# Kernel optimization log

Measured on AMD Instinct MI355X. Metric: run time of the kernel, lower is better.

## Reference

```python
import jax, jax.numpy as jnp
import numpy as np

D = 512
H = 2048
L = 8192
NSEG = 16
LN_EPS = 1e-6  # flax LayerNorm default


def _ln_tokens(x):
    # flax LayerNorm(reduction_axes=-2, feature_axes=-1, use_bias=False, use_scale=False):
    # mean/var reduced over the token axis (-2), per feature; no learned params.
    mu = jnp.mean(x, axis=-2, keepdims=True)
    var = jnp.var(x, axis=-2, keepdims=True)
    return (x - mu) * jax.lax.rsqrt(var + LN_EPS)


def setup_inputs() -> dict:
    key = jax.random.key(0)
    ks = jax.random.split(key, 8)
    xcat = jax.random.normal(ks[0], (L, D), dtype=jnp.float32)
    xsep = jnp.sort(jax.random.randint(ks[1], (L,), 0, NSEG)).astype(jnp.int64)
    s = 0.02
    Wqkv = jax.random.normal(ks[2], (D, 3 * D), dtype=jnp.float32) * s
    bqkv = jnp.zeros((3 * D,), dtype=jnp.float32)
    W1 = jax.random.normal(ks[3], (D, H), dtype=jnp.float32) * s
    b1 = jnp.zeros((H,), dtype=jnp.float32)
    W2 = jax.random.normal(ks[4], (H, D), dtype=jnp.float32) * s
    b2 = jnp.zeros((D,), dtype=jnp.float32)
    return {"xcat": xcat, "xsep": xsep, "Wqkv": Wqkv, "bqkv": bqkv,
            "W1": W1, "b1": b1, "W2": W2, "b2": b2}


def reference(xcat, xsep, Wqkv, bqkv, W1, b1, W2, b2):
    Ltok = xcat.shape[0]
    qkv = _ln_tokens(xcat) @ Wqkv + bqkv            # [L, 3D]
    q = qkv[:, :D]
    k = qkv[:, D:2 * D]
    # v = qkv[:, 2*D:3*D]  # computed in original but never used
    # unscaled scores; softmax FIRST, then mask, then renormalize (faithful to source)
    atten = jax.nn.softmax(jnp.einsum('id,jd->ij', q, k), axis=-1)  # [L, L]
    idx = jnp.arange(Ltok)
    mask = (xsep[None, :] == xsep[:, None]) & (idx[None, :] <= idx[:, None])
    atten = atten * mask
    atten = atten / (atten.sum(axis=-1, keepdims=True) + 1e-10)
    ctx = atten @ xcat                               # attention applied to raw xcat
    ffn = jax.nn.relu(_ln_tokens(ctx) @ W1 + b1) @ W2 + b2
    return (xcat + ffn, xsep)
```

## Files before the change

### kernel.cpp

```cpp
#include <hip/hip_runtime.h>
#include <math.h>

#define LTOK 8192
#define DDIM 512
#define HDIM 2048
#define NSEG 16
#define DCUT 32
#define ZROWS (NSEG * DCUT)
#define ZCH 64
#define NPART (ZCH * 4)
#define BM 128
#define BN 128
#define BK 64
#define PW 1280
#define PTILES (PW / BN)
#define ZGB (ZCH * (ZROWS / BM))
#define SPB (PTILES * 64)
#define ZG_PER (ZGB / 128)
#define SP_PER (SPB / 128)
#define GRP_SZ (ZG_PER + SP_PER)

typedef float f32x4 __attribute__((ext_vector_type(4)));
typedef short s16x8 __attribute__((ext_vector_type(8)));

static __device__ __forceinline__ short f2bf(float f) {
    union { float f; unsigned u; } v; v.f = f;
    unsigned r = (v.u + 0x7fffu + ((v.u >> 16) & 1u)) >> 16;
    return (short)r;
}
static __device__ __forceinline__ float bf2f(short s) {
    union { unsigned u; float f; } v;
    v.u = ((unsigned)(unsigned short)s) << 16;
    return v.f;
}

template<int GX, int GY>
__device__ __forceinline__ void swz_yslow(int& x, int& y) {
    constexpr int cpx = (GX * GY) >> 3;
    const int orig = blockIdx.y * GX + blockIdx.x;
    const int lg = (orig & 7) * cpx + (orig >> 3);
    y = lg / GX;
    x = lg - y * GX;
}

__global__ void ln_stats_partial(const float* __restrict__ X,
                                 float* __restrict__ psum, float* __restrict__ psumsq) {
    int c = threadIdx.x;
    int b = blockIdx.x;
    const float* p = X + (size_t)b * 256 * DDIM + c;
    float s = 0.f, s2 = 0.f;
    for (int r = 0; r < 256; ++r) {
        float v = p[(size_t)r * DDIM];
        s += v; s2 += v * v;
    }
    psum[b * DDIM + c] = s;
    psumsq[b * DDIM + c] = s2;
}

__global__ void ln_stats_final(const float* __restrict__ psum, const float* __restrict__ psumsq,
                               float* __restrict__ mu, float* __restrict__ rstd, int nb) {
    int c = threadIdx.x;
    float s = 0.f, s2 = 0.f;
    for (int b = 0; b < nb; ++b) { s += psum[b * DDIM + c]; s2 += psumsq[b * DDIM + c]; }
    float m = s / (float)LTOK;
    float var = s2 / (float)LTOK - m * m;
    mu[c] = m;
    rstd[c] = rsqrtf(var + 1e-6f);
}

__global__ void ln_apply_bf16(const float* __restrict__ X,
                              const float* __restrict__ mu, const float* __restrict__ rstd,
                              short* __restrict__ out) {
    int t = blockIdx.x * 256 + threadIdx.x;
    int base = t * 4;
    int c = base & (DDIM - 1);
    float4 v = *(const float4*)(X + base);
    short4 o;
    o.x = f2bf((v.x - mu[c + 0]) * rstd[c + 0]);
    o.y = f2bf((v.y - mu[c + 1]) * rstd[c + 1]);
    o.z = f2bf((v.z - mu[c + 2]) * rstd[c + 2]);
    o.w = f2bf((v.w - mu[c + 3]) * rstd[c + 3]);
    *(short4*)(out + base) = o;
}

__global__ void transpose_w(const float* __restrict__ W, int ldw, int n0,
                            short* __restrict__ WT, int R) {
    __shared__ short t[32][33];
    int nb = n0 + blockIdx.x * 32;
    int rb = blockIdx.y * 32;
    int tx = threadIdx.x & 31, ty = threadIdx.x >> 5;
    for (int rr = ty; rr < 32; rr += 8)
        t[rr][tx] = f2bf(W[(size_t)(rb + rr) * ldw + nb + tx]);
    __syncthreads();
    for (int rr = ty; rr < 32; rr += 8)
        WT[(size_t)(nb - n0 + rr) * R + rb + tx] = t[tx][rr];
}

__global__ void transpose_bf16(const float* __restrict__ X, short* __restrict__ XT) {
    __shared__ short t[32][33];
    int c0 = blockIdx.x * 32;
    int r0 = blockIdx.y * 32;
    int tx = threadIdx.x & 31, ty = threadIdx.x >> 5;
    for (int rr = ty; rr < 32; rr += 8)
        t[rr][tx] = f2bf(X[(size_t)(r0 + rr) * DDIM + c0 + tx]);
    __syncthreads();
    for (int rr = ty; rr < 32; rr += 8)
        XT[(size_t)(c0 + rr) * LTOK + r0 + tx] = t[tx][rr];
}

__global__ void seg_begin_k(const int* __restrict__ sep, int* __restrict__ begin,
                            float* __restrict__ out2) {
    int i = blockIdx.x * 256 + threadIdx.x;
    if (i < LTOK) {
        if (i == 0 || sep[i] != sep[i - 1]) begin[sep[i]] = i;
        out2[i] = (float)sep[i];
    }
}

__global__ void gather_qz(const short* __restrict__ qk, const int* __restrict__ sep,
                          const int* __restrict__ begin, short* __restrict__ qg) {
    const int gi = blockIdx.x;
    const int s = gi / DCUT, d = gi - s * DCUT;
    const int r = begin[s] + d;
    if ((unsigned)r < LTOK && sep[r] == s) {
        const short2* src = (const short2*)(qk + (size_t)r * 1024);
        short2* dst = (short2*)(qg + (size_t)gi * DDIM);
        dst[threadIdx.x] = src[threadIdx.x];
    }
}

__device__ __forceinline__ void stage_tile512(const short* __restrict__ src, int lda,
                                              short* lds, int tid) {
    const int wave = tid >> 6;
    const int lane = tid & 63;
    #pragma unroll
    for (int u = 0; u < 2; ++u) {
        const int c = u * 512 + wave * 64 + lane;
        const short* g = src + (size_t)(c >> 3) * lda + (c & 7) * 8;
        short* l = lds + (size_t)(u * 512 + wave * 64) * 8;
        __builtin_amdgcn_global_load_lds(
            (const __attribute__((address_space(1))) unsigned int*)g,
            (__attribute__((address_space(3))) unsigned int*)l,
            16, 0, 0);
    }
}

__device__ __forceinline__ void mma8_step(const short (*As)[BK], const short (*Bs)[BK],
                                          f32x4 acc[4][2], int wr, int wc, int grp, int lrow) {
    #pragma unroll
    for (int kk = 0; kk < 2; ++kk) {
        s16x8 af[4], bfr[2];
        #pragma unroll
        for (int f = 0; f < 4; ++f)
            af[f] = *(const s16x8*)&As[wr * 64 + f * 16 + lrow][grp * 8 + kk * 32];
        #pragma unroll
        for (int f = 0; f < 2; ++f)
            bfr[f] = *(const s16x8*)&Bs[wc * 32 + f * 16 + lrow][grp * 8 + kk * 32];
        #pragma unroll
        for (int fm = 0; fm < 4; ++fm)
            #pragma unroll
            for (int fn = 0; fn < 2; ++fn)
                acc[fm][fn] = __builtin_amdgcn_mfma_f32_16x16x32_bf16(
                    af[fm], bfr[fn], acc[fm][fn], 0, 0, 0);
    }
}

template<int EPI, int GX, int GY>
__global__ __launch_bounds__(512) void mm_bt8(const short* __restrict__ A, int lda,
        const short* __restrict__ BT, int ldb,
        const float* __restrict__ bias, const float* __restrict__ resid,
        float* __restrict__ Cf, short* __restrict__ Cb, int ldc, int K) {
    __shared__ short As[BM][BK];
    __shared__ short Bs[BN][BK];
    const int tid = threadIdx.x;
    const int wave = tid >> 6, lane = tid & 63, grp = lane >> 4, lrow = lane & 15;
    const int wr = wave >> 2, wc = wave & 3;
    int bx, by;
    swz_yslow<GX, GY>(bx, by);
    const int m0 = by * BM, n0 = bx * BN;
    if (EPI == 3) {
        A += (size_t)blockIdx.z * K;
        BT += (size_t)blockIdx.z * K;
    }
    f32x4 acc[4][2];
    #pragma unroll
    for (int a = 0; a < 4; ++a)
        #pragma unroll
        for (int b = 0; b < 2; ++b) acc[a][b] = (f32x4){0.f, 0.f, 0.f, 0.f};
    for (int k0 = 0; k0 < K; k0 += BK) {
        __syncthreads();
        stage_tile512(A + (size_t)m0 * lda + k0, lda, &As[0][0], tid);
        stage_tile512(BT + (size_t)n0 * ldb + k0, ldb, &Bs[0][0], tid);
        asm volatile("s_waitcnt vmcnt(0)" ::: "memory");
        __syncthreads();
        mma8_step(As, Bs, acc, wr, wc, grp, lrow);
    }
    #pragma unroll
    for (int fm = 0; fm < 4; ++fm) {
        #pragma unroll
        for (int i = 0; i < 4; ++i) {
            int row = m0 + wr * 64 + fm * 16 + grp * 4 + i;
            #pragma unroll
            for (int fn = 0; fn < 2; ++fn) {
                int col = n0 + wc * 32 + fn * 16 + lrow;
                float v = acc[fm][fn][i] + (EPI == 3 ? 0.f : bias[col]);
                if (EPI == 1) v = fmaxf(v, 0.f);
                if (EPI == 2) {
                    Cf[(size_t)row * ldc + col] = v + resid[(size_t)row * ldc + col];
                } else if (EPI == 3) {
                    Cb[(size_t)blockIdx.z * ((size_t)LTOK * ldc)
                       + (size_t)row * ldc + col] = f2bf(v);
                } else {
                    Cb[(size_t)row * ldc + col] = f2bf(v);
                }
            }
        }
    }
}

__global__ void ffn2_combine(const short* __restrict__ hp, const float* __restrict__ b2,
                             const float* __restrict__ xcat, float* __restrict__ out) {
    const int t = blockIdx.x * 256 + threadIdx.x;
    const int base = t * 4;
    const int c = base & (DDIM - 1);
    float4 r = *(const float4*)(xcat + base);
    float4 a;
    a.x = r.x + b2[c + 0];
    a.y = r.y + b2[c + 1];
    a.z = r.z + b2[c + 2];
    a.w = r.w + b2[c + 3];
    #pragma unroll
    for (int z = 0; z < 4; ++z) {
        short4 p = *(const short4*)(hp + (size_t)z * LTOK * DDIM + base);
        a.x += bf2f(p.x); a.y += bf2f(p.y); a.z += bf2f(p.z); a.w += bf2f(p.w);
    }
    *(float4*)(out + base) = a;
}

__global__ __launch_bounds__(512) void attn_zgsp(const short* __restrict__ qg,
        const short* __restrict__ qk,
        const int* __restrict__ sep, const int* __restrict__ begin,
        short* __restrict__ P, float* __restrict__ Zg) {
    __shared__ short As[BM][BK];
    __shared__ short Bs[BN][BK];
    const int tid = threadIdx.x;
    const int wave = tid >> 6, lane = tid & 63, grp = lane >> 4, lrow = lane & 15;
    const int wr = wave >> 2, wc = wave & 3;
    const int bid = blockIdx.x;
    const int grpi = bid / GRP_SZ, rem = bid - grpi * GRP_SZ;
    f32x4 acc[4][2];
    #pragma unroll
    for (int a = 0; a < 4; ++a)
        #pragma unroll
        for (int b = 0; b < 2; ++b) acc[a][b] = (f32x4){0.f, 0.f, 0.f, 0.f};

    if (rem < ZG_PER) {
        const int orig = grpi * ZG_PER + rem;
        constexpr int cpx = ZGB >> 3;
        const int lg = (orig & 7) * cpx + (orig >> 3);
        const int bx = lg / (ZROWS / BM);
        const int by = lg - bx * (ZROWS / BM);
        const int g0 = by * BM;
        const int j0 = bx * BN;
        for (int k0 = 0; k0 < DDIM; k0 += BK) {
            __syncthreads();
            stage_tile512(qg + (size_t)g0 * DDIM + k0, DDIM, &As[0][0], tid);
            stage_tile512(qk + (size_t)j0 * 1024 + 512 + k0, 1024, &Bs[0][0], tid);
            asm volatile("s_waitcnt vmcnt(0)" ::: "memory");
            __syncthreads();
            mma8_step(As, Bs, acc, wr, wc, grp, lrow);
        }
        #pragma unroll
        for (int idx = 0; idx < 16; ++idx) {
            float z = __expf(acc[idx >> 2][0][idx & 3]) + __expf(acc[idx >> 2][1][idx & 3]);
            #pragma unroll
            for (int off = 1; off < 16; off <<= 1) z += __shfl_xor(z, off, 16);
            if (lrow == 0) {
                const int gi = g0 + wr * 64 + (idx >> 2) * 16 + grp * 4 + (idx & 3);
                Zg[(size_t)gi * NPART + bx * 4 + wc] = z;
            }
        }
    } else {
        const int orig = grpi * SP_PER + (rem - ZG_PER);
        constexpr int cpx = SPB >> 3;
        const int lg = (orig & 7) * cpx + (orig >> 3);
        const int by = lg / PTILES;
        const int bx = lg - by * PTILES;
        const int m0 = by * BM;
        const int jb0 = begin[sep[m0]] & ~(BN - 1);
        const int j0 = jb0 + bx * BN;
        if (j0 >= m0 + BM) return;
        for (int k0 = 0; k0 < DDIM; k0 += BK) {
            __syncthreads();
            stage_tile512(qk + (size_t)m0 * 1024 + k0, 1024, &As[0][0], tid);
            stage_tile512(qk + (size_t)j0 * 1024 + 512 + k0, 1024, &Bs[0][0], tid);
            asm volatile("s_waitcnt vmcnt(0)" ::: "memory");
            __syncthreads();
            mma8_step(As, Bs, acc, wr, wc, grp, lrow);
        }
        #pragma unroll
        for (int fm = 0; fm < 4; ++fm) {
            #pragma unroll
            for (int i = 0; i < 4; ++i) {
                const int row = m0 + wr * 64 + fm * 16 + grp * 4 + i;
                const int jsr = begin[sep[row]];
                short* pr = P + (size_t)row * PW + (j0 - jb0) + wc * 32;
                #pragma unroll
                for (int fn = 0; fn < 2; ++fn) {
                    const int col = j0 + wc * 32 + fn * 16 + lrow;
                    const float ez = __expf(acc[fm][fn][i]);
                    pr[fn * 16 + lrow] = f2bf((col >= jsr && col <= row) ? ez : 0.f);
                }
            }
        }
    }
}

__global__ void einv_k(const short* __restrict__ P,
                       const int* __restrict__ sep, const int* __restrict__ begin,
                       const float* __restrict__ Zg, float* __restrict__ invE) {
    const int wv = threadIdx.x >> 6, lane = threadIdx.x & 63;
    const int r = blockIdx.x * 4 + wv;
    const int m0 = r & ~(BM - 1);
    const int jb0 = begin[sep[m0]] & ~(BN - 1);
    const int kw = m0 + BM - jb0;
    const int sr = sep[r];
    const int jsr = begin[sr];
    const short* Pr = P + (size_t)r * PW;
    float e = 0.f;
    for (int c = lane * 2; c < kw; c += 128) {
        short2 v = *(const short2*)(Pr + c);
        e += bf2f(v.x) + bf2f(v.y);
    }
    const int d = r - jsr;
    float z = 0.f;
    if (d < DCUT) {
        const float* zr = Zg + (size_t)(sr * DCUT + d) * NPART;
        #pragma unroll
        for (int c = 0; c < NPART / 64; ++c) z += zr[c * 64 + lane];
    }
    #pragma unroll
    for (int off = 1; off < 64; off <<= 1) {
        e += __shfl_xor(e, off);
        z += __shfl_xor(z, off);
    }
    if (lane == 0) invE[r] = 1.f / (e + 1e-10f * z);
}

__global__ __launch_bounds__(512) void attn_pv(const short* __restrict__ P,
        const short* __restrict__ xbT,
        const int* __restrict__ sep, const int* __restrict__ begin,
        const float* __restrict__ invE, float* __restrict__ ctx,
        float* __restrict__ psum2, float* __restrict__ psumsq2) {
    __shared__ short As[BM][BK];
    __shared__ short Bs[BN][BK];
    __shared__ float Sacc[128][2];
    const int tid = threadIdx.x;
    const int wave = tid >> 6, lane = tid & 63, grp = lane >> 4, lrow = lane & 15;
    const int wr = wave >> 2, wc = wave & 3;
    int bx, by;
    swz_yslow<4, 64>(bx, by);
    const int m0 = by * BM, n0 = bx * BN;
    const int jbase0 = begin[sep[m0]] & ~(BN - 1);
    const int kmax = m0 + BM - jbase0;
    f32x4 acc[4][2];
    #pragma unroll
    for (int a = 0; a < 4; ++a)
        #pragma unroll
        for (int b = 0; b < 2; ++b) acc[a][b] = (f32x4){0.f, 0.f, 0.f, 0.f};
    for (int k0 = 0; k0 < kmax; k0 += BK) {
        __syncthreads();
        stage_tile512(P + (size_t)m0 * PW + k0, PW, &As[0][0], tid);
        stage_tile512(xbT + (size_t)n0 * LTOK + jbase0 + k0, LTOK, &Bs[0][0], tid);
        asm volatile("s_waitcnt vmcnt(0)" ::: "memory");
        __syncthreads();
        mma8_step(As, Bs, acc, wr, wc, grp, lrow);
    }
    if (tid < 128) { Sacc[tid][0] = 0.f; Sacc[tid][1] = 0.f; }
    __syncthreads();
    float cs[2] = {0.f, 0.f}, cq[2] = {0.f, 0.f};
    #pragma unroll
    for (int fm = 0; fm < 4; ++fm) {
        #pragma unroll
        for (int i = 0; i < 4; ++i) {
            int row = m0 + wr * 64 + fm * 16 + grp * 4 + i;
            float inv = invE[row];
            #pragma unroll
            for (int fn = 0; fn < 2; ++fn) {
                int col = n0 + wc * 32 + fn * 16 + lrow;
                float v = acc[fm][fn][i] * inv;
                ctx[(size_t)row * DDIM + col] = v;
                cs[fn] += v;
                cq[fn] += v * v;
            }
        }
    }
    #pragma unroll
    for (int fn = 0; fn < 2; ++fn) {
        cs[fn] += __shfl_xor(cs[fn], 16); cs[fn] += __shfl_xor(cs[fn], 32);
        cq[fn] += __shfl_xor(cq[fn], 16); cq[fn] += __shfl_xor(cq[fn], 32);
    }
    if (grp == 0) {
        #pragma unroll
        for (int fn = 0; fn < 2; ++fn) {
            const int cb = wc * 32 + fn * 16 + lrow;
            atomicAdd(&Sacc[cb][0], cs[fn]);
            atomicAdd(&Sacc[cb][1], cq[fn]);
        }
    }
    __syncthreads();
    if (tid < 128) {
        psum2[(size_t)by * DDIM + n0 + tid] = Sacc[tid][0];
        psumsq2[(size_t)by * DDIM + n0 + tid] = Sacc[tid][1];
    }
}

extern "C" void kernel_launch(void* const* d_in, const int* in_sizes, int n_in,
                              void* d_out, int out_size, void* d_ws, size_t ws_size,
                              hipStream_t stream) {
    const float* xcat = (const float*)d_in[0];
    const int* sep = (const int*)d_in[1];
    const float* Wqkv = (const float*)d_in[2];
    const float* bqkv = (const float*)d_in[3];
    const float* W1 = (const float*)d_in[4];
    const float* b1 = (const float*)d_in[5];
    const float* W2 = (const float*)d_in[6];
    const float* b2 = (const float*)d_in[7];
    float* out = (float*)d_out;

    float* ws = (float*)d_ws;
    float* psum    = ws;
    float* psumsq  = psum + 32 * DDIM;
    float* psum2   = psumsq + 32 * DDIM;
    float* psumsq2 = psum2 + 64 * DDIM;
    float* mu1     = psumsq2 + 64 * DDIM;
    float* rstd1   = mu1 + DDIM;
    float* mu2     = rstd1 + DDIM;
    float* rstd2   = mu2 + DDIM;
    float* invE    = rstd2 + DDIM;
    float* Zg      = invE + LTOK;
    int*   begin   = (int*)(Zg + (size_t)ZROWS * NPART);
    short* qg      = (short*)(begin + 1024);
    short* qk      = qg    + (size_t)ZROWS * DDIM;
    short* xbT     = qk    + (size_t)LTOK * 1024;
    short* lnx     = xbT   + (size_t)DDIM * LTOK;
    short* lnctx   = lnx   + (size_t)LTOK * DDIM;
    short* hb      = lnctx + (size_t)LTOK * DDIM;
    short* Pbuf    = hb;
    short* WqkvT   = hb    + (size_t)LTOK * HDIM;
    short* W1T     = WqkvT + (size_t)1024 * DDIM;
    short* W2T     = W1T   + (size_t)HDIM * DDIM;
    float* ctxF    = (float*)(W2T + (size_t)DDIM * HDIM);
    short* hpart   = qk;

    ln_stats_partial<<<dim3(32), dim3(512), 0, stream>>>(xcat, psum, psumsq);
    ln_stats_final<<<dim3(1), dim3(512), 0, stream>>>(psum, psumsq, mu1, rstd1, 32);
    ln_apply_bf16<<<dim3(LTOK * DDIM / 4 / 256), dim3(256), 0, stream>>>(xcat, mu1, rstd1, lnx);

    transpose_w<<<dim3(32, 16), dim3(256), 0, stream>>>(Wqkv, 3 * DDIM, 0, WqkvT, DDIM);
    transpose_w<<<dim3(64, 16), dim3(256), 0, stream>>>(W1, HDIM, 0, W1T, DDIM);
    transpose_w<<<dim3(16, 64), dim3(256), 0, stream>>>(W2, DDIM, 0, W2T, HDIM);

    mm_bt8<0, 8, 64><<<dim3(8, 64), dim3(512), 0, stream>>>(
        lnx, DDIM, WqkvT, DDIM, bqkv, (const float*)nullptr,
        (float*)nullptr, qk, 1024, DDIM);

    seg_begin_k<<<dim3(32), dim3(256), 0, stream>>>(sep, begin, out + (size_t)LTOK * DDIM);
    transpose_bf16<<<dim3(16, 256), dim3(256), 0, stream>>>(xcat, xbT);

    gather_qz<<<dim3(ZROWS), dim3(256), 0, stream>>>(qk, sep, begin, qg);
    attn_zgsp<<<dim3(ZGB + SPB), dim3(512), 0, stream>>>(qg, qk, sep, begin, Pbuf, Zg);

    einv_k<<<dim3(LTOK / 4), dim3(256), 0, stream>>>(Pbuf, sep, begin, Zg, invE);
    attn_pv<<<dim3(4, 64), dim3(512), 0, stream>>>(Pbuf, xbT, sep, begin, invE, ctxF,
                                                   psum2, psumsq2);

    ln_stats_final<<<dim3(1), dim3(512), 0, stream>>>(psum2, psumsq2, mu2, rstd2, 64);
    ln_apply_bf16<<<dim3(LTOK * DDIM / 4 / 256), dim3(256), 0, stream>>>(ctxF, mu2, rstd2, lnctx);

    mm_bt8<1, 16, 64><<<dim3(16, 64), dim3(512), 0, stream>>>(
        lnctx, DDIM, W1T, DDIM, b1, (const float*)nullptr,
        (float*)nullptr, hb, HDIM, DDIM);

    mm_bt8<3, 4, 64><<<dim3(4, 64, 4), dim3(512), 0, stream>>>(
        hb, HDIM, W2T, HDIM, (const float*)nullptr, (const float*)nullptr,
        (float*)nullptr, hpart, DDIM, HDIM / 4);
    ffn2_combine<<<dim3(LTOK * DDIM / 4 / 256), dim3(256), 0, stream>>>(hpart, b2, xcat, out);
}
```

Measured before the change: 216.9 us.

## Use double-buffered 256x256 tile GEMM for the FFN matmuls

Adds a new GEMM kernel with 256x256 output tiles per block and double-buffered LDS staging, so the next K-slice loads while MFMAs run on the current one. FFN1 and FFN2 now use it in place of the 128x128 single-buffered kernel. The larger tiles raise operand reuse and cut global traffic. In exchange each thread holds 128 accumulator floats, LDS use grows to 128KB per block, and grids shrink to 256 blocks, which may hurt occupancy and load balance across CUs.

```diff
diff --git a/kernel.cpp b/kernel.cpp
--- a/kernel.cpp
+++ b/kernel.cpp
@@ -145,6 +145,22 @@
     }
 }
 
+__device__ __forceinline__ void stage_tile256(const short* __restrict__ src, int lda,
+                                              short* lds, int tid) {
+    const int wave = tid >> 6;
+    const int lane = tid & 63;
+    #pragma unroll
+    for (int u = 0; u < 4; ++u) {
+        const int c = u * 512 + wave * 64 + lane;
+        const short* g = src + (size_t)(c >> 3) * lda + (c & 7) * 8;
+        short* l = lds + (size_t)(u * 512 + wave * 64) * 8;
+        __builtin_amdgcn_global_load_lds(
+            (const __attribute__((address_space(1))) unsigned int*)g,
+            (__attribute__((address_space(3))) unsigned int*)l,
+            16, 0, 0);
+    }
+}
+
 __device__ __forceinline__ void mma8_step(const short (*As)[BK], const short (*Bs)[BK],
                                           f32x4 acc[4][2], int wr, int wc, int grp, int lrow) {
     #pragma unroll
@@ -203,6 +219,87 @@
             #pragma unroll
             for (int fn = 0; fn < 2; ++fn) {
                 int col = n0 + wc * 32 + fn * 16 + lrow;
+                float v = acc[fm][fn][i] + (EPI == 3 ? 0.f : bias[col]);
+                if (EPI == 1) v = fmaxf(v, 0.f);
+                if (EPI == 2) {
+                    Cf[(size_t)row * ldc + col] = v + resid[(size_t)row * ldc + col];
+                } else if (EPI == 3) {
+                    Cb[(size_t)blockIdx.z * ((size_t)LTOK * ldc)
+                       + (size_t)row * ldc + col] = f2bf(v);
+                } else {
+                    Cb[(size_t)row * ldc + col] = f2bf(v);
+                }
+            }
+        }
+    }
+}
+
+template<int EPI, int GX, int GY>
+__global__ __launch_bounds__(512) void mm_bt256p(const short* __restrict__ A, int lda,
+        const short* __restrict__ BT, int ldb,
+        const float* __restrict__ bias, const float* __restrict__ resid,
+        float* __restrict__ Cf, short* __restrict__ Cb, int ldc, int K) {
+    __shared__ short As[2][256][BK];
+    __shared__ short Bs[2][256][BK];
+    const int tid = threadIdx.x;
+    const int wave = tid >> 6, lane = tid & 63, grp = lane >> 4, lrow = lane & 15;
+    const int wr = wave >> 2, wc = wave & 3;
+    int bx, by;
+    swz_yslow<GX, GY>(bx, by);
+    const int m0 = by * 256, n0 = bx * 256;
+    if (EPI == 3) {
+        A += (size_t)blockIdx.z * K;
+        BT += (size_t)blockIdx.z * K;
+    }
+    f32x4 acc[8][4];
+    #pragma unroll
+    for (int a = 0; a < 8; ++a)
+        #pragma unroll
+        for (int b = 0; b < 4; ++b) acc[a][b] = (f32x4){0.f, 0.f, 0.f, 0.f};
+
+    stage_tile256(A + (size_t)m0 * lda, lda, &As[0][0][0], tid);
+    stage_tile256(BT + (size_t)n0 * ldb, ldb, &Bs[0][0][0], tid);
+    asm volatile("s_waitcnt vmcnt(0)" ::: "memory");
+    __builtin_amdgcn_s_barrier();
+
+    const int nsteps = K / BK;
+    int cur = 0;
+    for (int s = 0; s < nsteps; ++s) {
+        if (s + 1 < nsteps) {
+            stage_tile256(A + (size_t)m0 * lda + (s + 1) * BK, lda, &As[cur ^ 1][0][0], tid);
+            stage_tile256(BT + (size_t)n0 * ldb + (s + 1) * BK, ldb, &Bs[cur ^ 1][0][0], tid);
+        }
+        #pragma unroll
+        for (int kk = 0; kk < 2; ++kk) {
+            s16x8 af[8], bfr[4];
+            #pragma unroll
+            for (int f = 0; f < 8; ++f)
+                af[f] = *(const s16x8*)&As[cur][wr * 128 + f * 16 + lrow][grp * 8 + kk * 32];
+            #pragma unroll
+            for (int f = 0; f < 4; ++f)
+                bfr[f] = *(const s16x8*)&Bs[cur][wc * 64 + f * 16 + lrow][grp * 8 + kk * 32];
+            #pragma unroll
+            for (int fm = 0; fm < 8; ++fm)
+                #pragma unroll
+                for (int fn = 0; fn < 4; ++fn)
+                    acc[fm][fn] = __builtin_amdgcn_mfma_f32_16x16x32_bf16(
+                        af[fm], bfr[fn], acc[fm][fn], 0, 0, 0);
+        }
+        __builtin_amdgcn_sched_barrier(0);
+        asm volatile("s_waitcnt vmcnt(0)" ::: "memory");
+        __builtin_amdgcn_sched_barrier(0);
+        __builtin_amdgcn_s_barrier();
+        cur ^= 1;
+    }
+
+    #pragma unroll
+    for (int fm = 0; fm < 8; ++fm) {
+        #pragma unroll
+        for (int i = 0; i < 4; ++i) {
+            int row = m0 + wr * 128 + fm * 16 + grp * 4 + i;
+            #pragma unroll
+            for (int fn = 0; fn < 4; ++fn) {
+                int col = n0 + wc * 64 + fn * 16 + lrow;
                 float v = acc[fm][fn][i] + (EPI == 3 ? 0.f : bias[col]);
                 if (EPI == 1) v = fmaxf(v, 0.f);
                 if (EPI == 2) {
@@ -478,11 +575,11 @@
     ln_stats_final<<<dim3(1), dim3(512), 0, stream>>>(psum2, psumsq2, mu2, rstd2, 64);
     ln_apply_bf16<<<dim3(LTOK * DDIM / 4 / 256), dim3(256), 0, stream>>>(ctxF, mu2, rstd2, lnctx);
 
-    mm_bt8<1, 16, 64><<<dim3(16, 64), dim3(512), 0, stream>>>(
+    mm_bt256p<1, 8, 32><<<dim3(8, 32), dim3(512), 0, stream>>>(
         lnctx, DDIM, W1T, DDIM, b1, (const float*)nullptr,
         (float*)nullptr, hb, HDIM, DDIM);
 
-    mm_bt8<3, 4, 64><<<dim3(4, 64, 4), dim3(512), 0, stream>>>(
+    mm_bt256p<3, 2, 32><<<dim3(2, 32, 4), dim3(512), 0, stream>>>(
         hb, HDIM, W2T, HDIM, (const float*)nullptr, (const float*)nullptr,
         (float*)nullptr, hpart, DDIM, HDIM / 4);
     ffn2_combine<<<dim3(LTOK * DDIM / 4 / 256), dim3(256), 0, stream>>>(hpart, b2, xcat, out);
```

Measured after the change: 217.0 us. Within noise of the previous version (+0.0%).
